# Kernel tuning notes

Hardware: AMD Instinct MI355X
Metric: run time of the kernel (lower is better)

The kernel has to match this reference:

```python
import jax, jax.numpy as jnp
import numpy as np

B, NR, IC, NC, OC = 64, 16384, 16, 10, 16
NUM_ITERS = 3


def setup_inputs() -> dict:
    key = jax.random.key(0)
    k1, k2, k3, k4 = jax.random.split(key, 4)
    x = jax.random.normal(k1, (B, NR, IC), dtype=jnp.float32)
    W = jax.random.normal(k2, (IC, NC, OC, NR), dtype=jnp.float32)
    fc_w = jax.random.normal(k3, (1, NC * OC), dtype=jnp.float32)
    fc_b = jax.random.normal(k4, (1,), dtype=jnp.float32)
    return {"x": x, "W": W, "fc_w": fc_w, "fc_b": fc_b}


def _squash(s):
    # Original squash is applied to tensors with trailing dim of size 1,
    # so the norm reduction is elementwise: s^2 * s / ((1+s^2) * sqrt(s^2))
    sq = s * s
    return sq * s / ((1.0 + sq) * jnp.sqrt(sq))


def reference(x, W, fc_w, fc_b):
    batch = x.shape[0]
    in_ch, nc, oc, nr = W.shape
    # u_hat[b,i,c,o] = sum_r W[i,c,o,r] * x[b,r,i]  (x is identical across capsules)
    u_hat = jnp.einsum('icor,bri->bico', W, x)  # [B, in_ch, nc, oc]
    b_ij = jnp.zeros((in_ch, nc), dtype=x.dtype)
    v_j = None
    for it in range(NUM_ITERS):
        c_ij = jax.nn.softmax(b_ij, axis=0)              # softmax over in_channels
        s_j = jnp.einsum('ic,bico->bco', c_ij, u_hat)    # [B, nc, oc]
        v_j = _squash(s_j)
        if it < NUM_ITERS - 1:
            # agreement a[b,i,c] = sum_o u_hat[b,i,c,o] * v[b,c,o]; mean over batch
            a_ij = jnp.einsum('bico,bco->ic', u_hat, v_j) / batch
            b_ij = b_ij + a_ij
    pred = jax.nn.sigmoid(v_j.reshape(batch, -1) @ fc_w.T + fc_b)[:, 0]  # [B]
    return pred, v_j[..., None]  # v_j returned as [B, nc, oc, 1] like torch
```

## Files before the change

kernel.cpp:

```cpp
#include <hip/hip_runtime.h>

typedef unsigned int uint;
typedef unsigned short ushort;
typedef __attribute__((ext_vector_type(8))) short bf16x8;
typedef __attribute__((ext_vector_type(4))) float floatx4;

#define B_   64
#define NR_  16384
#define IC_  16
#define NC_  10
#define OC_  16
#define NCO  160
#define KC_  32
#define KT_  32
#define NSTEP 16

__device__ __forceinline__ float bf2f(ushort h) {
    return __uint_as_float(((uint)h) << 16);
}
__device__ __forceinline__ ushort f2bf(float f) {
    uint u = __float_as_uint(f);
    u += 0x7fffu + ((u >> 16) & 1u);
    return (ushort)(u >> 16);
}
__device__ __forceinline__ void splitbf(float f, ushort& h, ushort& l) {
    h = f2bf(f);
    l = f2bf(f - bf2f(h));
}
__device__ __forceinline__ float squashf(float s) {
    return s * fabsf(s) / (1.0f + s * s);
}

__global__ __launch_bounds__(256) void k_xT(const float* __restrict__ xf,
                                            ushort* __restrict__ xTh,
                                            ushort* __restrict__ xTl,
                                            float* __restrict__ uh)
{
    const int chunk = blockIdx.x, b = blockIdx.y, t = threadIdx.x;
    if (chunk == 0) {
        float4 z = {0.f, 0.f, 0.f, 0.f};
        float4* dst = (float4*)(uh + (size_t)b * (IC_ * NCO));
        for (int n = t; n < 640; n += 256) dst[n] = z;
    }
    const int r0 = chunk * 1024;
#pragma unroll
    for (int j = 0; j < 4; ++j) {
        int r = r0 + t + 256 * j;
        const float* row = xf + ((size_t)b * NR_ + r) * IC_;
        float vals[16];
        *(float4*)&vals[0]  = *(const float4*)row;
        *(float4*)&vals[4]  = *(const float4*)(row + 4);
        *(float4*)&vals[8]  = *(const float4*)(row + 8);
        *(float4*)&vals[12] = *(const float4*)(row + 12);
#pragma unroll
        for (int i = 0; i < 16; ++i) {
            ushort h, l;
            splitbf(vals[i], h, l);
            size_t idx = ((size_t)(i * B_ + b)) * NR_ + r;
            xTh[idx] = h;
            xTl[idx] = l;
        }
    }
}

__device__ __forceinline__ void loadW5(const float* __restrict__ wbase_st,
                                       int tid, float2* r)
{
#pragma unroll
    for (int s = 0; s < 5; ++s) {
        int idx2 = tid + 512 * s;
        int row  = idx2 >> 4;
        int e    = idx2 & 15;
        r[s] = *(const float2*)(wbase_st + (size_t)row * NR_ + 2 * e);
    }
}

__device__ __forceinline__ void storeW5(const float2* r, int tid,
                                        ushort* __restrict__ WhB,
                                        ushort* __restrict__ WlB)
{
#pragma unroll
    for (int s = 0; s < 5; ++s) {
        int idx2 = tid + 512 * s;
        int row  = idx2 >> 4;
        int e    = idx2 & 15;
        ushort h0, l0, h1, l1;
        splitbf(r[s].x, h0, l0);
        splitbf(r[s].y, h1, l1);
        *(uint*)&WhB[row * 40 + 2 * e] = (uint)h0 | ((uint)h1 << 16);
        *(uint*)&WlB[row * 40 + 2 * e] = (uint)l0 | ((uint)l1 << 16);
    }
}

__device__ __forceinline__ void loadX(const ushort* __restrict__ xTh,
                                      const ushort* __restrict__ xTl,
                                      size_t xrow, int st, int has_xt,
                                      const float* __restrict__ xf,
                                      int b, int i, int r0, int quad,
                                      bf16x8& h, bf16x8& l)
{
    if (has_xt) {
        size_t o = xrow + (size_t)st * KT_;
        h = *(const bf16x8*)&xTh[o];
        l = *(const bf16x8*)&xTl[o];
    } else {
#pragma unroll
        for (int q = 0; q < 8; ++q) {
            float v = xf[((size_t)b * NR_ + r0 + st * KT_ + quad * 8 + q) * IC_ + i];
            ushort hh, ll;
            splitbf(v, hh, ll);
            h[q] = (short)hh;
            l[q] = (short)ll;
        }
    }
}

__device__ __forceinline__ void mfma5(const ushort* __restrict__ WhB,
                                      const ushort* __restrict__ WlB,
                                      bf16x8 ah, bf16x8 al,
                                      floatx4* acc, int cg, int m16, int quad)
{
#pragma unroll
    for (int t5 = 0; t5 < 5; ++t5) {
        int corow = (cg * 5 + t5) * 16 + m16;
        bf16x8 bh = *(const bf16x8*)&WhB[corow * 40 + quad * 8];
        bf16x8 bl = *(const bf16x8*)&WlB[corow * 40 + quad * 8];
        acc[t5] = __builtin_amdgcn_mfma_f32_16x16x32_bf16(ah, bh, acc[t5], 0, 0, 0);
        acc[t5] = __builtin_amdgcn_mfma_f32_16x16x32_bf16(al, bh, acc[t5], 0, 0, 0);
        acc[t5] = __builtin_amdgcn_mfma_f32_16x16x32_bf16(ah, bl, acc[t5], 0, 0, 0);
    }
}

__global__ __launch_bounds__(512, 4) void k_uhat(const float* __restrict__ xf,
                                                 const float* __restrict__ wf,
                                                 const ushort* __restrict__ xTh,
                                                 const ushort* __restrict__ xTl,
                                                 int has_xt,
                                                 float* __restrict__ uh)
{
    const int i    = blockIdx.x;
    const int kc   = blockIdx.y;
    const int tid  = threadIdx.x;
    const int lane = tid & 63;
    const int w    = tid >> 6;
    const int quad = lane >> 4;
    const int m16  = lane & 15;
    const int bt   = w & 3;
    const int cg   = w >> 2;

    __shared__ ushort Wh[2][160 * 40];
    __shared__ ushort Wl[2][160 * 40];

    floatx4 acc[5];
#pragma unroll
    for (int t = 0; t < 5; ++t) acc[t] = (floatx4){0.f, 0.f, 0.f, 0.f};

    const int r0 = kc * (NR_ / KC_);
    const float* wbase = wf + (size_t)i * NCO * NR_ + r0;
    const int xb = bt * 16 + m16;
    const size_t xrow = (size_t)(i * B_ + xb) * NR_ + r0 + quad * 8;

    float2 wA[5], wB[5];
    bf16x8 xhA, xlA, xhB, xlB;

    loadW5(wbase, tid, wA);
    loadX(xTh, xTl, xrow, 0, has_xt, xf, xb, i, r0, quad, xhA, xlA);
    storeW5(wA, tid, Wh[0], Wl[0]);
    loadW5(wbase + 1 * KT_, tid, wB);
    __syncthreads();

    for (int st = 0; st < NSTEP; st += 2) {
        loadX(xTh, xTl, xrow, st + 1, has_xt, xf, xb, i, r0, quad, xhB, xlB);
        storeW5(wB, tid, Wh[1], Wl[1]);
        if (st + 2 < NSTEP) loadW5(wbase + (size_t)(st + 2) * KT_, tid, wA);
        mfma5(Wh[0], Wl[0], xhA, xlA, acc, cg, m16, quad);
        __syncthreads();

        if (st + 2 < NSTEP) {
            loadX(xTh, xTl, xrow, st + 2, has_xt, xf, xb, i, r0, quad, xhA, xlA);
            storeW5(wA, tid, Wh[0], Wl[0]);
        }
        if (st + 3 < NSTEP) loadW5(wbase + (size_t)(st + 3) * KT_, tid, wB);
        mfma5(Wh[1], Wl[1], xhB, xlB, acc, cg, m16, quad);
        __syncthreads();
    }

#pragma unroll
    for (int t5 = 0; t5 < 5; ++t5) {
        int co = (cg * 5 + t5) * 16 + m16;
#pragma unroll
        for (int r = 0; r < 4; ++r) {
            int b = bt * 16 + quad * 4 + r;
            atomicAdd(&uh[(b * IC_ + i) * NCO + co], acc[t5][r]);
        }
    }
}

__global__ __launch_bounds__(256) void k_route(const float* __restrict__ uh,
                                               const float* __restrict__ fcw,
                                               const float* __restrict__ fcb,
                                               float* __restrict__ out)
{
    const int bo = blockIdx.x, t = threadIdx.x;
    __shared__ float vL[B_ * NCO];
    __shared__ float a1L[160];
    __shared__ float bL[160];
    __shared__ float cL[160];

    for (int q4 = t; q4 < 2560; q4 += 256) {
        int b = q4 / 40, r = q4 - b * 40;
        const float4* up = (const float4*)(uh + (size_t)b * 2560 + r * 4);
        float4 s = {0.f, 0.f, 0.f, 0.f};
#pragma unroll
        for (int i2 = 0; i2 < 16; ++i2) {
            float4 u4 = up[i2 * 40];
            s.x += u4.x; s.y += u4.y; s.z += u4.z; s.w += u4.w;
        }
        float4 v;
        v.x = squashf(s.x * 0.0625f);
        v.y = squashf(s.y * 0.0625f);
        v.z = squashf(s.z * 0.0625f);
        v.w = squashf(s.w * 0.0625f);
        *((float4*)vL + q4) = v;
    }
    __syncthreads();
    if (t < 160) {
        int c = t >> 4, i2 = t & 15;
        const float* up0 = uh + i2 * NCO + c * 16;
        const float* vp0 = vL + c * 16;
        float4 s4 = {0.f, 0.f, 0.f, 0.f};
        for (int b = 0; b < 64; ++b) {
            const float4* up = (const float4*)(up0 + (size_t)b * 2560);
            const float4* vp = (const float4*)(vp0 + b * 160);
#pragma unroll
            for (int q = 0; q < 4; ++q) {
                float4 u4 = up[q], v4 = vp[q];
                s4.x += u4.x * v4.x; s4.y += u4.y * v4.y;
                s4.z += u4.z * v4.z; s4.w += u4.w * v4.w;
            }
        }
        a1L[t] = ((s4.x + s4.y) + (s4.z + s4.w)) * (1.0f / 64.0f);
    }
    __syncthreads();
    if (t < 160) {
        int c = t >> 4;
        float m = -1e30f;
#pragma unroll
        for (int i2 = 0; i2 < 16; ++i2) m = fmaxf(m, a1L[c * 16 + i2]);
        float Z = 0.f;
#pragma unroll
        for (int i2 = 0; i2 < 16; ++i2) Z += expf(a1L[c * 16 + i2] - m);
        cL[t] = expf(a1L[t] - m) / Z;
    }
    __syncthreads();
    for (int q4 = t; q4 < 2560; q4 += 256) {
        int b = q4 / 40, r = q4 - b * 40;
        int c = r >> 2;
        const float4* up = (const float4*)(uh + (size_t)b * 2560 + r * 4);
        float4 s = {0.f, 0.f, 0.f, 0.f};
#pragma unroll
        for (int i2 = 0; i2 < 16; ++i2) {
            float w2 = cL[c * 16 + i2];
            float4 u4 = up[i2 * 40];
            s.x += w2 * u4.x; s.y += w2 * u4.y;
            s.z += w2 * u4.z; s.w += w2 * u4.w;
        }
        float4 v;
        v.x = squashf(s.x); v.y = squashf(s.y);
        v.z = squashf(s.z); v.w = squashf(s.w);
        *((float4*)vL + q4) = v;
    }
    __syncthreads();
    if (t < 160) {
        int c = t >> 4, i2 = t & 15;
        const float* up0 = uh + i2 * NCO + c * 16;
        const float* vp0 = vL + c * 16;
        float4 s4 = {0.f, 0.f, 0.f, 0.f};
        for (int b = 0; b < 64; ++b) {
            const float4* up = (const float4*)(up0 + (size_t)b * 2560);
            const float4* vp = (const float4*)(vp0 + b * 160);
#pragma unroll
            for (int q = 0; q < 4; ++q) {
                float4 u4 = up[q], v4 = vp[q];
                s4.x += u4.x * v4.x; s4.y += u4.y * v4.y;
                s4.z += u4.z * v4.z; s4.w += u4.w * v4.w;
            }
        }
        bL[t] = a1L[t] + ((s4.x + s4.y) + (s4.z + s4.w)) * (1.0f / 64.0f);
    }
    __syncthreads();
    if (t < 160) {
        int c = t >> 4;
        float m = -1e30f;
#pragma unroll
        for (int i2 = 0; i2 < 16; ++i2) m = fmaxf(m, bL[c * 16 + i2]);
        float Z = 0.f;
#pragma unroll
        for (int i2 = 0; i2 < 16; ++i2) Z += expf(bL[c * 16 + i2] - m);
        cL[t] = expf(bL[t] - m) / Z;
    }
    __syncthreads();
    if (t < 160) {
        int c = t >> 4;
        const float* ub = uh + (size_t)bo * 2560 + t;
        float s = 0.f;
#pragma unroll
        for (int i2 = 0; i2 < 16; ++i2) s += cL[c * 16 + i2] * ub[i2 * NCO];
        float v = squashf(s);
        out[64 + bo * NCO + t] = v;
        bL[t] = v * fcw[t];
    }
    __syncthreads();
    if (t == 0) {
        float a = fcb[0];
        for (int j = 0; j < 160; ++j) a += bL[j];
        out[bo] = 1.0f / (1.0f + expf(-a));
    }
}

extern "C" void kernel_launch(void* const* d_in, const int* in_sizes, int n_in,
                              void* d_out, int out_size, void* d_ws, size_t ws_size,
                              hipStream_t stream)
{
    const float* x   = (const float*)d_in[0];
    const float* W   = (const float*)d_in[1];
    const float* fcw = (const float*)d_in[2];
    const float* fcb = (const float*)d_in[3];
    float* out = (float*)d_out;

    float* uh = (float*)d_ws;
    const size_t xt_off   = 1u << 20;
    const size_t xt_bytes = (size_t)IC_ * B_ * NR_ * 2;
    ushort* xTh = (ushort*)((char*)d_ws + xt_off);
    ushort* xTl = (ushort*)((char*)d_ws + xt_off + xt_bytes);
    const int has_xt = (ws_size >= xt_off + 2 * xt_bytes) ? 1 : 0;

    if (has_xt) {
        k_xT<<<dim3(16, 64), 256, 0, stream>>>(x, xTh, xTl, uh);
    } else {
        hipMemsetAsync(uh, 0, (size_t)(B_ * IC_ * NCO) * sizeof(float), stream);
    }
    k_uhat<<<dim3(IC_, KC_), 512, 0, stream>>>(x, W, xTh, xTl, has_xt, uh);
    k_route<<<B_, 256, 0, stream>>>(uh, fcw, fcb, out);
}
```

Baseline: 355.7 us.

## Stage x tiles in shared memory and single-buffer W with register prefetch

Replaces the double-buffered W shared tiles and per-wave direct x loads with a single-buffered scheme. Each k-step, x hi/lo planes are loaded once per block into shared memory, so the two wave groups no longer fetch the same x rows twice. The next step's W and x are prefetched into registers. This cuts shared memory and redundant global x traffic and drops the occupancy hint from launch_bounds. In exchange it needs two barriers per step with no LDS double-buffering, so compute and LDS stores serialize more.

```diff
diff --git a/kernel.cpp b/kernel.cpp
--- a/kernel.cpp
+++ b/kernel.cpp
@@ -4,6 +4,7 @@
 typedef unsigned short ushort;
 typedef __attribute__((ext_vector_type(8))) short bf16x8;
 typedef __attribute__((ext_vector_type(4))) float floatx4;
+typedef __attribute__((ext_vector_type(4))) uint uint4v;
 
 #define B_   64
 #define NR_  16384
@@ -92,51 +93,12 @@
     }
 }
 
-__device__ __forceinline__ void loadX(const ushort* __restrict__ xTh,
-                                      const ushort* __restrict__ xTl,
-                                      size_t xrow, int st, int has_xt,
-                                      const float* __restrict__ xf,
-                                      int b, int i, int r0, int quad,
-                                      bf16x8& h, bf16x8& l)
-{
-    if (has_xt) {
-        size_t o = xrow + (size_t)st * KT_;
-        h = *(const bf16x8*)&xTh[o];
-        l = *(const bf16x8*)&xTl[o];
-    } else {
-#pragma unroll
-        for (int q = 0; q < 8; ++q) {
-            float v = xf[((size_t)b * NR_ + r0 + st * KT_ + quad * 8 + q) * IC_ + i];
-            ushort hh, ll;
-            splitbf(v, hh, ll);
-            h[q] = (short)hh;
-            l[q] = (short)ll;
-        }
-    }
-}
-
-__device__ __forceinline__ void mfma5(const ushort* __restrict__ WhB,
-                                      const ushort* __restrict__ WlB,
-                                      bf16x8 ah, bf16x8 al,
-                                      floatx4* acc, int cg, int m16, int quad)
-{
-#pragma unroll
-    for (int t5 = 0; t5 < 5; ++t5) {
-        int corow = (cg * 5 + t5) * 16 + m16;
-        bf16x8 bh = *(const bf16x8*)&WhB[corow * 40 + quad * 8];
-        bf16x8 bl = *(const bf16x8*)&WlB[corow * 40 + quad * 8];
-        acc[t5] = __builtin_amdgcn_mfma_f32_16x16x32_bf16(ah, bh, acc[t5], 0, 0, 0);
-        acc[t5] = __builtin_amdgcn_mfma_f32_16x16x32_bf16(al, bh, acc[t5], 0, 0, 0);
-        acc[t5] = __builtin_amdgcn_mfma_f32_16x16x32_bf16(ah, bl, acc[t5], 0, 0, 0);
-    }
-}
-
-__global__ __launch_bounds__(512, 4) void k_uhat(const float* __restrict__ xf,
-                                                 const float* __restrict__ wf,
-                                                 const ushort* __restrict__ xTh,
-                                                 const ushort* __restrict__ xTl,
-                                                 int has_xt,
-                                                 float* __restrict__ uh)
+__global__ __launch_bounds__(512) void k_uhat(const float* __restrict__ xf,
+                                              const float* __restrict__ wf,
+                                              const ushort* __restrict__ xTh,
+                                              const ushort* __restrict__ xTl,
+                                              int has_xt,
+                                              float* __restrict__ uh)
 {
     const int i    = blockIdx.x;
     const int kc   = blockIdx.y;
@@ -148,8 +110,8 @@
     const int bt   = w & 3;
     const int cg   = w >> 2;
 
-    __shared__ ushort Wh[2][160 * 40];
-    __shared__ ushort Wl[2][160 * 40];
+    __shared__ ushort Xh[64 * 40], Xl[64 * 40];
+    __shared__ ushort Wh[160 * 40], Wl[160 * 40];
 
     floatx4 acc[5];
 #pragma unroll
@@ -157,34 +119,58 @@
 
     const int r0 = kc * (NR_ / KC_);
     const float* wbase = wf + (size_t)i * NCO * NR_ + r0;
-    const int xb = bt * 16 + m16;
-    const size_t xrow = (size_t)(i * B_ + xb) * NR_ + r0 + quad * 8;
-
-    float2 wA[5], wB[5];
-    bf16x8 xhA, xlA, xhB, xlB;
-
-    loadW5(wbase, tid, wA);
-    loadX(xTh, xTl, xrow, 0, has_xt, xf, xb, i, r0, quad, xhA, xlA);
-    storeW5(wA, tid, Wh[0], Wl[0]);
-    loadW5(wbase + 1 * KT_, tid, wB);
-    __syncthreads();
-
-    for (int st = 0; st < NSTEP; st += 2) {
-        loadX(xTh, xTl, xrow, st + 1, has_xt, xf, xb, i, r0, quad, xhB, xlB);
-        storeW5(wB, tid, Wh[1], Wl[1]);
-        if (st + 2 < NSTEP) loadW5(wbase + (size_t)(st + 2) * KT_, tid, wA);
-        mfma5(Wh[0], Wl[0], xhA, xlA, acc, cg, m16, quad);
+
+    const int t8 = tid & 255, bb = t8 >> 2, part = t8 & 3;
+    const ushort* xplane = (tid < 256) ? xTh : xTl;
+    ushort* xdst = (tid < 256) ? &Xh[bb * 40 + part * 8] : &Xl[bb * 40 + part * 8];
+    const size_t xsrc0 = (size_t)(i * B_ + bb) * NR_ + r0 + part * 8;
+
+    float2 wr[5];
+    uint4v xr;
+
+    loadW5(wbase, tid, wr);
+    if (has_xt) xr = *(const uint4v*)&xplane[xsrc0];
+
+    for (int st = 0; st < NSTEP; ++st) {
+        const int rb = r0 + st * KT_;
+        float2 wc[5];
+#pragma unroll
+        for (int s = 0; s < 5; ++s) wc[s] = wr[s];
+        uint4v xc = xr;
+        if (st + 1 < NSTEP) {
+            loadW5(wbase + (size_t)(st + 1) * KT_, tid, wr);
+            if (has_xt) xr = *(const uint4v*)&xplane[xsrc0 + (size_t)(st + 1) * KT_];
+        }
+
         __syncthreads();
-
-        if (st + 2 < NSTEP) {
-            loadX(xTh, xTl, xrow, st + 2, has_xt, xf, xb, i, r0, quad, xhA, xlA);
-            storeW5(wA, tid, Wh[0], Wl[0]);
-        }
-        if (st + 3 < NSTEP) loadW5(wbase + (size_t)(st + 3) * KT_, tid, wB);
-        mfma5(Wh[1], Wl[1], xhB, xlB, acc, cg, m16, quad);
+        if (has_xt) {
+            *(uint4v*)xdst = xc;
+        } else {
+#pragma unroll
+            for (int s = 0; s < 4; ++s) {
+                int n = tid + 512 * s;
+                int bb2 = n >> 5, k = n & 31;
+                float v = xf[(size_t)bb2 * (NR_ * IC_) + (size_t)(rb + k) * IC_ + i];
+                ushort h, l;
+                splitbf(v, h, l);
+                Xh[bb2 * 40 + k] = h;
+                Xl[bb2 * 40 + k] = l;
+            }
+        }
+        storeW5(wc, tid, Wh, Wl);
         __syncthreads();
-    }
-
+        bf16x8 afh = *(const bf16x8*)&Xh[(bt * 16 + m16) * 40 + quad * 8];
+        bf16x8 afl = *(const bf16x8*)&Xl[(bt * 16 + m16) * 40 + quad * 8];
+#pragma unroll
+        for (int t5 = 0; t5 < 5; ++t5) {
+            int corow = (cg * 5 + t5) * 16 + m16;
+            bf16x8 bh = *(const bf16x8*)&Wh[corow * 40 + quad * 8];
+            bf16x8 bl = *(const bf16x8*)&Wl[corow * 40 + quad * 8];
+            acc[t5] = __builtin_amdgcn_mfma_f32_16x16x32_bf16(afh, bh, acc[t5], 0, 0, 0);
+            acc[t5] = __builtin_amdgcn_mfma_f32_16x16x32_bf16(afl, bh, acc[t5], 0, 0, 0);
+            acc[t5] = __builtin_amdgcn_mfma_f32_16x16x32_bf16(afh, bl, acc[t5], 0, 0, 0);
+        }
+    }
 #pragma unroll
     for (int t5 = 0; t5 < 5; ++t5) {
         int co = (cg * 5 + t5) * 16 + m16;
```

Result: no change. 353.6 us (-0.6%).
